# Optimization experiments

Hardware: AMD Instinct MI355X
Metric: run time of the kernel (lower is better)

## Reference

```python
import jax, jax.numpy as jnp
import numpy as np

WS = 8            # window size
N = WS * WS       # tokens per window
C = 192           # in_features
H = 6             # heads
HD = C // H       # head dim
MH = 256          # meta network hidden
BW = 4096         # batch_size * windows
NW_MASK = 64      # number of mask window patterns


def _relative_coords_log():
    idx = np.arange(WS)
    coords = np.stack(np.meshgrid(idx, idx, indexing='ij'), axis=0).reshape(2, -1)  # [2, N]
    rel = coords[:, :, None] - coords[:, None, :]            # [2, N, N]
    rel = rel.transpose(1, 2, 0).reshape(-1, 2).astype(np.float32)  # [N*N, 2]
    return jnp.asarray(np.sign(rel) * np.log1p(np.abs(rel)))


def setup_inputs() -> dict:
    key = jax.random.key(0)
    ks = jax.random.split(key, 12)
    s = 0.02
    return {
        'x': jax.random.normal(ks[0], (BW, C, WS, WS), jnp.float32),
        'mask': jax.random.normal(ks[1], (NW_MASK, N, N), jnp.float32),
        'W_qkv': jax.random.normal(ks[2], (C, 3 * C), jnp.float32) * s,
        'b_qkv': jnp.zeros((3 * C,), jnp.float32),
        'W_proj': jax.random.normal(ks[3], (C, C), jnp.float32) * s,
        'b_proj': jnp.zeros((C,), jnp.float32),
        'mW1': jax.random.normal(ks[4], (2, MH), jnp.float32) * 0.1,
        'mb1': jnp.zeros((MH,), jnp.float32),
        'mW2': jax.random.normal(ks[5], (MH, H), jnp.float32) * 0.1,
        'mb2': jnp.zeros((H,), jnp.float32),
        'tau': jnp.ones((H,), jnp.float32),
    }


def _l2norm(v):
    n = jnp.sqrt(jnp.sum(v * v, axis=-1, keepdims=True))
    return v / jnp.maximum(n, 1e-12)


def reference(x, mask, W_qkv, b_qkv, W_proj, b_proj, mW1, mb1, mW2, mb2, tau):
    Bw = x.shape[0]
    # [Bw, C, ws, ws] -> tokens [Bw, N, C]
    tokens = x.reshape(Bw, C, N).transpose(0, 2, 1)
    qkv = tokens @ W_qkv + b_qkv                                  # [Bw, N, 3C]
    qkv = qkv.reshape(Bw, N, 3, H, HD).transpose(2, 0, 3, 1, 4)   # [3, Bw, H, N, HD]
    q, k, v = qkv[0], qkv[1], qkv[2]
    # scaled cosine attention
    attn = jnp.einsum('bhnd,bhmd->bhnm', _l2norm(q), _l2norm(k))
    attn = attn / jnp.clip(tau, 0.01, None)[None, :, None, None]
    # continuous relative position bias via meta network
    rel_log = _relative_coords_log()                              # [N*N, 2]
    bias = jax.nn.relu(rel_log @ mW1 + mb1) @ mW2 + mb2           # [N*N, H]
    bias = bias.T.reshape(H, N, N)
    attn = attn + bias[None]
    # shifted-window mask, pattern indexed by window id modulo nW_mask
    idx = jnp.arange(Bw) % mask.shape[0]
    attn = attn + mask[idx][:, None]                              # [Bw, 1, N, N]
    attn = jax.nn.softmax(attn, axis=-1)
    out = jnp.einsum('bhnm,bhmd->bhnd', attn, v)
    out = out.transpose(0, 2, 1, 3).reshape(Bw, N, C)
    out = out @ W_proj + b_proj
    # back to [Bw, C, ws, ws]
    return out.transpose(0, 2, 1).reshape(Bw, C, WS, WS)
```

## Files before the change

kernel.cpp:

```cpp
#include <hip/hip_runtime.h>

typedef _Float16 f16;
typedef _Float16 f16x2 __attribute__((ext_vector_type(2)));
typedef _Float16 f16x4 __attribute__((ext_vector_type(4)));
typedef _Float16 f16x8 __attribute__((ext_vector_type(8)));
typedef float f32x4 __attribute__((ext_vector_type(4)));

#define NT 64
#define CH 192
#define NH 6
#define MH 256
#define BWIN 4096
#define LOG2E 1.44269504f

#define STOK 200
#define SMEM_BYTES 49152

#define MFMA16(a, b, c) __builtin_amdgcn_mfma_f32_16x16x16f16(a, b, c, 0, 0, 0)
#define MFMA32(a, b, c) __builtin_amdgcn_mfma_f32_16x16x32_f16(a, b, c, 0, 0, 0)

__device__ __forceinline__ int qkidx(int n, int d) {
    return n * 32 + ((((d >> 3) + (n >> 1)) & 3) << 3) + (d & 7);
}

__global__ void bias_kernel(const float* __restrict__ mW1, const float* __restrict__ mb1,
                            const float* __restrict__ mW2, const float* __restrict__ mb2,
                            float* __restrict__ bias_tbl) {
    int p = blockIdx.x * blockDim.x + threadIdx.x;
    if (p >= NT * NT) return;
    int n = p >> 6, m = p & 63;
    float di = (float)((n >> 3) - (m >> 3));
    float dj = (float)((n & 7) - (m & 7));
    float r0 = copysignf(log1pf(fabsf(di)), di);
    float r1 = copysignf(log1pf(fabsf(dj)), dj);
    float acc[NH];
#pragma unroll
    for (int h = 0; h < NH; h++) acc[h] = mb2[h];
    for (int k = 0; k < MH; k++) {
        float hv = fmaxf(r0 * mW1[k] + r1 * mW1[MH + k] + mb1[k], 0.0f);
#pragma unroll
        for (int h = 0; h < NH; h++) acc[h] += hv * mW2[k * NH + h];
    }
#pragma unroll
    for (int h = 0; h < NH; h++) bias_tbl[h * (NT * NT) + p] = acc[h];
}

__global__ void prep_kernel(const float* __restrict__ Wqkv, const float* __restrict__ Wproj,
                            f16* __restrict__ Wpk, f16* __restrict__ Wpp) {
    int i = blockIdx.x * blockDim.x + threadIdx.x;
    const int NQ = 36 * 6 * 64 * 8;
    if (i < NQ) {
        int t = i & 7, lane = (i >> 3) & 63, ks = (i >> 9) % 6, ct = i >> 9; ct /= 6;
        int o = 16 * ct + (lane & 15);
        int c = ks * 32 + (lane >> 4) * 8 + t;
        Wpk[i] = (f16)Wqkv[c * 576 + o];
    } else if (i < NQ + 12 * 6 * 64 * 8) {
        int j = i - NQ;
        int t = j & 7, lane = (j >> 3) & 63, ks = (j >> 9) % 6, ct = j >> 9; ct /= 6;
        int o = 16 * ct + (lane & 15);
        int c = ks * 32 + (lane >> 4) * 8 + t;
        Wpp[j] = (f16)Wproj[c * 192 + o];
    }
}

__global__ void comb_kernel(const float* __restrict__ mask, const float* __restrict__ bias_tbl,
                            float* __restrict__ comb) {
    int j = blockIdx.x * blockDim.x + threadIdx.x;
    if (j >= 64 * NH * NT * NT) return;
    int im = j / (NH * NT * NT);
    int rem = j % (NH * NT * NT);
    int h = rem >> 12;
    int p = rem & 4095;
    comb[j] = (mask[im * 4096 + p] + bias_tbl[h * 4096 + p]) * LOG2E;
}

__launch_bounds__(384)
__global__ void attn_kernel(const float* __restrict__ x, const float* __restrict__ bqkv,
                            const float* __restrict__ bproj, const float* __restrict__ tau,
                            const f16* __restrict__ Wpk, const f16* __restrict__ Wpp,
                            const float* __restrict__ comb, float* __restrict__ out) {
    __shared__ __align__(16) char smem[SMEM_BYTES];
    f16* tok = (f16*)smem;
    f16* qk  = (f16*)smem;
    f16* ao  = (f16*)smem;

    const int b   = blockIdx.x;
    const int tid = threadIdx.x;
    const int l   = tid & 63;
    const int w   = __builtin_amdgcn_readfirstlane(tid >> 6);
    const int c16 = l & 15;
    const int g4  = l >> 4;

    {
        const float* xb = x + (size_t)b * (CH * NT);
        const int n4 = 4 * c16;
#pragma unroll
        for (int i = 0; i < 4; i++) {
            int c = 32 * w + 8 * g4 + 2 * i;
            f32x4 a0 = *(const f32x4*)(xb + c * NT + n4);
            f32x4 a1 = *(const f32x4*)(xb + (c + 1) * NT + n4);
#pragma unroll
            for (int j = 0; j < 4; j++) {
                f16x2 p;
                p[0] = (f16)a0[j];
                p[1] = (f16)a1[j];
                *(f16x2*)(tok + (n4 + j) * STOK + c) = p;
            }
        }
    }
    __syncthreads();

    f16x4 hq[2][4], hk[2][4];
    {
        f32x4 aq_[2][4] = {};
#pragma unroll
        for (int ks = 0; ks < 6; ks++) {
            f16x8 af[4];
#pragma unroll
            for (int nt = 0; nt < 4; nt++)
                af[nt] = *(const f16x8*)(tok + (16 * nt + c16) * STOK + ks * 32 + 8 * g4);
#pragma unroll
            for (int dt = 0; dt < 2; dt++) {
                f16x8 wf = *(const f16x8*)(Wpk + (((size_t)(2 * w + dt) * 6 + ks) * 64 + l) * 8);
#pragma unroll
                for (int nt = 0; nt < 4; nt++)
                    aq_[dt][nt] = MFMA32(wf, af[nt], aq_[dt][nt]);
            }
        }
#pragma unroll
        for (int dt = 0; dt < 2; dt++) {
            f32x4 bb = *(const f32x4*)(bqkv + 32 * w + 16 * dt + 4 * g4);
#pragma unroll
            for (int nt = 0; nt < 4; nt++)
#pragma unroll
                for (int r = 0; r < 4; r++) aq_[dt][nt][r] += bb[r];
        }
#pragma unroll
        for (int nt = 0; nt < 4; nt++) {
            float ss = 0.f;
#pragma unroll
            for (int dt = 0; dt < 2; dt++)
#pragma unroll
                for (int r = 0; r < 4; r++) ss += aq_[dt][nt][r] * aq_[dt][nt][r];
            ss += __shfl_xor(ss, 16);
            ss += __shfl_xor(ss, 32);
            float iq = 1.0f / fmaxf(sqrtf(ss), 1e-12f);
#pragma unroll
            for (int dt = 0; dt < 2; dt++)
#pragma unroll
                for (int r = 0; r < 4; r++) hq[dt][nt][r] = (f16)(aq_[dt][nt][r] * iq);
        }
    }
    {
        f32x4 ak_[2][4] = {};
#pragma unroll
        for (int ks = 0; ks < 6; ks++) {
            f16x8 af[4];
#pragma unroll
            for (int nt = 0; nt < 4; nt++)
                af[nt] = *(const f16x8*)(tok + (16 * nt + c16) * STOK + ks * 32 + 8 * g4);
#pragma unroll
            for (int dt = 0; dt < 2; dt++) {
                f16x8 wf = *(const f16x8*)(Wpk + (((size_t)(12 + 2 * w + dt) * 6 + ks) * 64 + l) * 8);
#pragma unroll
                for (int nt = 0; nt < 4; nt++)
                    ak_[dt][nt] = MFMA32(wf, af[nt], ak_[dt][nt]);
            }
        }
#pragma unroll
        for (int dt = 0; dt < 2; dt++) {
            f32x4 bb = *(const f32x4*)(bqkv + 192 + 32 * w + 16 * dt + 4 * g4);
#pragma unroll
            for (int nt = 0; nt < 4; nt++)
#pragma unroll
                for (int r = 0; r < 4; r++) ak_[dt][nt][r] += bb[r];
        }
#pragma unroll
        for (int nt = 0; nt < 4; nt++) {
            float ss = 0.f;
#pragma unroll
            for (int dt = 0; dt < 2; dt++)
#pragma unroll
                for (int r = 0; r < 4; r++) ss += ak_[dt][nt][r] * ak_[dt][nt][r];
            ss += __shfl_xor(ss, 16);
            ss += __shfl_xor(ss, 32);
            float ik = 1.0f / fmaxf(sqrtf(ss), 1e-12f);
#pragma unroll
            for (int dt = 0; dt < 2; dt++)
#pragma unroll
                for (int r = 0; r < 4; r++) hk[dt][nt][r] = (f16)(ak_[dt][nt][r] * ik);
        }
    }
    f16x4 vb[2][4];
    {
        f32x4 av_[2][4] = {};
#pragma unroll
        for (int ks = 0; ks < 6; ks++) {
            f16x8 af[4];
#pragma unroll
            for (int mt = 0; mt < 4; mt++)
                af[mt] = *(const f16x8*)(tok + (16 * mt + c16) * STOK + ks * 32 + 8 * g4);
#pragma unroll
            for (int dt = 0; dt < 2; dt++) {
                f16x8 wf = *(const f16x8*)(Wpk + (((size_t)(24 + 2 * w + dt) * 6 + ks) * 64 + l) * 8);
#pragma unroll
                for (int mt = 0; mt < 4; mt++)
                    av_[dt][mt] = MFMA32(af[mt], wf, av_[dt][mt]);
            }
        }
#pragma unroll
        for (int dt = 0; dt < 2; dt++) {
            float bb = bqkv[384 + 32 * w + 16 * dt + c16];
#pragma unroll
            for (int mt = 0; mt < 4; mt++)
#pragma unroll
                for (int r = 0; r < 4; r++) vb[dt][mt][r] = (f16)(av_[dt][mt][r] + bb);
        }
    }

    __syncthreads();

    f16* qh = qk + (w * 2 + 0) * 2048;
    f16* kh = qk + (w * 2 + 1) * 2048;
#pragma unroll
    for (int nt = 0; nt < 4; nt++)
#pragma unroll
        for (int dt = 0; dt < 2; dt++) {
            int base = qkidx(16 * nt + c16, 16 * dt + 4 * g4);
            f16x2 p;
            p[0] = hq[dt][nt][0]; p[1] = hq[dt][nt][1];
            *(f16x2*)(qh + base) = p;
            p[0] = hq[dt][nt][2]; p[1] = hq[dt][nt][3];
            *(f16x2*)(qh + base + 2) = p;
            p[0] = hk[dt][nt][0]; p[1] = hk[dt][nt][1];
            *(f16x2*)(kh + base) = p;
            p[0] = hk[dt][nt][2]; p[1] = hk[dt][nt][3];
            *(f16x2*)(kh + base + 2) = p;
        }

    f32x4 sv[4][4];
    {
        f16x8 aqf[4];
#pragma unroll
        for (int t = 0; t < 4; t++)
            aqf[t] = *(const f16x8*)(qh + qkidx(16 * t + c16, 8 * g4));
#pragma unroll
        for (int mt = 0; mt < 4; mt++) {
            f16x8 akf = *(const f16x8*)(kh + qkidx(16 * mt + c16, 8 * g4));
#pragma unroll
            for (int nt = 0; nt < 4; nt++) {
                f32x4 z = {};
                sv[mt][nt] = MFMA32(akf, aqf[nt], z);
            }
        }
    }

    {
        const float itau_l2 = LOG2E / fmaxf(tau[w], 0.01f);
        const float* cb = comb + ((size_t)((b & 63) * NH + w)) * (NT * NT);
#pragma unroll
        for (int mt = 0; mt < 4; mt++)
#pragma unroll
            for (int nt = 0; nt < 4; nt++) {
                f32x4 cc = *(const f32x4*)(cb + (16 * nt + c16) * NT + 16 * mt + 4 * g4);
#pragma unroll
                for (int r = 0; r < 4; r++)
                    sv[mt][nt][r] = sv[mt][nt][r] * itau_l2 + cc[r];
            }
    }

#pragma unroll
    for (int nt = 0; nt < 4; nt++) {
        float mx = sv[0][nt][0];
#pragma unroll
        for (int mt = 0; mt < 4; mt++)
#pragma unroll
            for (int r = 0; r < 4; r++) mx = fmaxf(mx, sv[mt][nt][r]);
        mx = fmaxf(mx, __shfl_xor(mx, 16));
        mx = fmaxf(mx, __shfl_xor(mx, 32));
        float sum = 0.f;
#pragma unroll
        for (int mt = 0; mt < 4; mt++)
#pragma unroll
            for (int r = 0; r < 4; r++) {
                float p = exp2f(sv[mt][nt][r] - mx);
                sv[mt][nt][r] = p;
                sum += p;
            }
        sum += __shfl_xor(sum, 16);
        sum += __shfl_xor(sum, 32);
        float ris = 1.0f / sum;
#pragma unroll
        for (int mt = 0; mt < 4; mt++)
#pragma unroll
            for (int r = 0; r < 4; r++) sv[mt][nt][r] *= ris;
    }

    f16x4 pa[4][4];
#pragma unroll
    for (int mk = 0; mk < 4; mk++)
#pragma unroll
        for (int nt = 0; nt < 4; nt++) {
            f16x4 h;
#pragma unroll
            for (int r = 0; r < 4; r++) h[r] = (f16)sv[mk][nt][r];
            pa[mk][nt] = h;
        }

    f32x4 av[4][2] = {};
#pragma unroll
    for (int mk = 0; mk < 4; mk++)
#pragma unroll
        for (int nt = 0; nt < 4; nt++)
#pragma unroll
            for (int dt = 0; dt < 2; dt++)
                av[nt][dt] = MFMA16(pa[mk][nt], vb[dt][mk], av[nt][dt]);

    __syncthreads();

#pragma unroll
    for (int nt = 0; nt < 4; nt++)
#pragma unroll
        for (int dt = 0; dt < 2; dt++)
#pragma unroll
            for (int r = 0; r < 4; r++)
                ao[(16 * nt + 4 * g4 + r) * STOK + 32 * w + 16 * dt + c16] = (f16)av[nt][dt][r];
    __syncthreads();

    f32x4 acc2[2][4] = {};
#pragma unroll
    for (int ks = 0; ks < 6; ks++) {
        f16x8 af[4];
#pragma unroll
        for (int rt = 0; rt < 4; rt++)
            af[rt] = *(const f16x8*)(ao + (16 * rt + c16) * STOK + ks * 32 + 8 * g4);
#pragma unroll
        for (int c2 = 0; c2 < 2; c2++) {
            f16x8 bw = *(const f16x8*)(Wpp + (((size_t)(2 * w + c2) * 6 + ks) * 64 + l) * 8);
#pragma unroll
            for (int rt = 0; rt < 4; rt++)
                acc2[c2][rt] = MFMA32(af[rt], bw, acc2[c2][rt]);
        }
    }
    float* ob = out + (size_t)b * (CH * NT);
#pragma unroll
    for (int c2 = 0; c2 < 2; c2++) {
        int c = 16 * (2 * w + c2) + c16;
        float bp = bproj[c];
#pragma unroll
        for (int rt = 0; rt < 4; rt++) {
            f32x4 o4 = acc2[c2][rt];
            o4[0] += bp; o4[1] += bp; o4[2] += bp; o4[3] += bp;
            *(f32x4*)(ob + c * NT + 16 * rt + 4 * g4) = o4;
        }
    }
}

#define WS_BIAS 0
#define WS_WPK  98304
#define WS_WPP  319488
#define WS_COMB 393216

extern "C" void kernel_launch(void* const* d_in, const int* in_sizes, int n_in,
                              void* d_out, int out_size, void* d_ws, size_t ws_size,
                              hipStream_t stream) {
    const float* x     = (const float*)d_in[0];
    const float* mask  = (const float*)d_in[1];
    const float* Wqkv  = (const float*)d_in[2];
    const float* bqkv  = (const float*)d_in[3];
    const float* Wproj = (const float*)d_in[4];
    const float* bproj = (const float*)d_in[5];
    const float* mW1   = (const float*)d_in[6];
    const float* mb1   = (const float*)d_in[7];
    const float* mW2   = (const float*)d_in[8];
    const float* mb2   = (const float*)d_in[9];
    const float* tau   = (const float*)d_in[10];

    char* ws = (char*)d_ws;
    float* bias_tbl = (float*)(ws + WS_BIAS);
    f16*   Wpk      = (f16*)(ws + WS_WPK);
    f16*   Wpp      = (f16*)(ws + WS_WPP);
    float* comb     = (float*)(ws + WS_COMB);

    bias_kernel<<<16, 256, 0, stream>>>(mW1, mb1, mW2, mb2, bias_tbl);
    int prep_n = 36 * 6 * 64 * 8 + 12 * 6 * 64 * 8;
    prep_kernel<<<(prep_n + 255) / 256, 256, 0, stream>>>(Wqkv, Wproj, Wpk, Wpp);
    int comb_n = 64 * NH * NT * NT;
    comb_kernel<<<(comb_n + 255) / 256, 256, 0, stream>>>(mask, bias_tbl, comb);
    attn_kernel<<<BWIN, 384, 0, stream>>>(x, bqkv, bproj, tau, Wpk, Wpp, comb,
                                          (float*)d_out);
}
```

Before: 338.4 us.

## Process two windows per block to reuse weight fragments across windows

```diff
diff --git a/kernel.cpp b/kernel.cpp
--- a/kernel.cpp
+++ b/kernel.cpp
@@ -14,7 +14,8 @@
 #define LOG2E 1.44269504f
 
 #define STOK 200
-#define SMEM_BYTES 49152
+#define WIN_BYTES 49152
+#define SMEM_BYTES (2 * WIN_BYTES)
 
 #define MFMA16(a, b, c) __builtin_amdgcn_mfma_f32_16x16x16f16(a, b, c, 0, 0, 0)
 #define MFMA32(a, b, c) __builtin_amdgcn_mfma_f32_16x16x32_f16(a, b, c, 0, 0, 0)
@@ -74,284 +75,291 @@
     comb[j] = (mask[im * 4096 + p] + bias_tbl[h * 4096 + p]) * LOG2E;
 }
 
+template <bool TRANS>
+__device__ __forceinline__ void qkv_pass(const f16* tokA, const f16* tokB,
+                                         const f16* __restrict__ Wpk, int ctbase,
+                                         int c16, int g4, int l,
+                                         f32x4 (&accA)[2][4], f32x4 (&accB)[2][4]) {
+#pragma unroll
+    for (int ks = 0; ks < 6; ks++) {
+        f16x8 afA[4], afB[4];
+#pragma unroll
+        for (int nt = 0; nt < 4; nt++) {
+            afA[nt] = *(const f16x8*)(tokA + (16 * nt + c16) * STOK + ks * 32 + 8 * g4);
+            afB[nt] = *(const f16x8*)(tokB + (16 * nt + c16) * STOK + ks * 32 + 8 * g4);
+        }
+#pragma unroll
+        for (int dt = 0; dt < 2; dt++) {
+            f16x8 wf = *(const f16x8*)(Wpk + (((size_t)(ctbase + dt) * 6 + ks) * 64 + l) * 8);
+#pragma unroll
+            for (int nt = 0; nt < 4; nt++) {
+                if (TRANS) {
+                    accA[dt][nt] = MFMA32(wf, afA[nt], accA[dt][nt]);
+                    accB[dt][nt] = MFMA32(wf, afB[nt], accB[dt][nt]);
+                } else {
+                    accA[dt][nt] = MFMA32(afA[nt], wf, accA[dt][nt]);
+                    accB[dt][nt] = MFMA32(afB[nt], wf, accB[dt][nt]);
+                }
+            }
+        }
+    }
+}
+
+__device__ __forceinline__ void norm_pack(const f32x4 (&acc)[2][4], const float* __restrict__ bq,
+                                          int w, int g4, f16x4 (&h)[2][4]) {
+    f32x4 bb0 = *(const f32x4*)(bq + 32 * w + 4 * g4);
+    f32x4 bb1 = *(const f32x4*)(bq + 32 * w + 16 + 4 * g4);
+#pragma unroll
+    for (int nt = 0; nt < 4; nt++) {
+        float a0[4], a1[4];
+        float ss = 0.f;
+#pragma unroll
+        for (int r = 0; r < 4; r++) {
+            a0[r] = acc[0][nt][r] + bb0[r];
+            a1[r] = acc[1][nt][r] + bb1[r];
+            ss += a0[r] * a0[r] + a1[r] * a1[r];
+        }
+        ss += __shfl_xor(ss, 16);
+        ss += __shfl_xor(ss, 32);
+        float inv = 1.0f / fmaxf(sqrtf(ss), 1e-12f);
+#pragma unroll
+        for (int r = 0; r < 4; r++) {
+            h[0][nt][r] = (f16)(a0[r] * inv);
+            h[1][nt][r] = (f16)(a1[r] * inv);
+        }
+    }
+}
+
+__device__ __forceinline__ void attn_one(const f16* qh, const f16* kh,
+                                         const float* __restrict__ cb, float itau_l2,
+                                         const f16x4 (&vb)[2][4], int c16, int g4,
+                                         f32x4 (&av)[4][2]) {
+    f32x4 sv[4][4];
+    {
+        f16x8 aqf[4];
+#pragma unroll
+        for (int t = 0; t < 4; t++)
+            aqf[t] = *(const f16x8*)(qh + qkidx(16 * t + c16, 8 * g4));
+#pragma unroll
+        for (int mt = 0; mt < 4; mt++) {
+            f16x8 akf = *(const f16x8*)(kh + qkidx(16 * mt + c16, 8 * g4));
+#pragma unroll
+            for (int nt = 0; nt < 4; nt++) {
+                f32x4 z = {};
+                sv[mt][nt] = MFMA32(akf, aqf[nt], z);
+            }
+        }
+    }
+#pragma unroll
+    for (int mt = 0; mt < 4; mt++)
+#pragma unroll
+        for (int nt = 0; nt < 4; nt++) {
+            f32x4 cc = *(const f32x4*)(cb + (16 * nt + c16) * NT + 16 * mt + 4 * g4);
+#pragma unroll
+            for (int r = 0; r < 4; r++)
+                sv[mt][nt][r] = sv[mt][nt][r] * itau_l2 + cc[r];
+        }
+#pragma unroll
+    for (int nt = 0; nt < 4; nt++) {
+        float mx = sv[0][nt][0];
+#pragma unroll
+        for (int mt = 0; mt < 4; mt++)
+#pragma unroll
+            for (int r = 0; r < 4; r++) mx = fmaxf(mx, sv[mt][nt][r]);
+        mx = fmaxf(mx, __shfl_xor(mx, 16));
+        mx = fmaxf(mx, __shfl_xor(mx, 32));
+        float sum = 0.f;
+#pragma unroll
+        for (int mt = 0; mt < 4; mt++)
+#pragma unroll
+            for (int r = 0; r < 4; r++) {
+                float p = exp2f(sv[mt][nt][r] - mx);
+                sv[mt][nt][r] = p;
+                sum += p;
+            }
+        sum += __shfl_xor(sum, 16);
+        sum += __shfl_xor(sum, 32);
+        float ris = 1.0f / sum;
+#pragma unroll
+        for (int mt = 0; mt < 4; mt++)
+#pragma unroll
+            for (int r = 0; r < 4; r++) sv[mt][nt][r] *= ris;
+    }
+    f16x4 pa[4][4];
+#pragma unroll
+    for (int mk = 0; mk < 4; mk++)
+#pragma unroll
+        for (int nt = 0; nt < 4; nt++) {
+            f16x4 h;
+#pragma unroll
+            for (int r = 0; r < 4; r++) h[r] = (f16)sv[mk][nt][r];
+            pa[mk][nt] = h;
+        }
+#pragma unroll
+    for (int nt = 0; nt < 4; nt++)
+#pragma unroll
+        for (int dt = 0; dt < 2; dt++) {
+            f32x4 z = {};
+            av[nt][dt] = z;
+        }
+#pragma unroll
+    for (int mk = 0; mk < 4; mk++)
+#pragma unroll
+        for (int nt = 0; nt < 4; nt++)
+#pragma unroll
+            for (int dt = 0; dt < 2; dt++)
+                av[nt][dt] = MFMA16(pa[mk][nt], vb[dt][mk], av[nt][dt]);
+}
+
 __launch_bounds__(384)
 __global__ void attn_kernel(const float* __restrict__ x, const float* __restrict__ bqkv,
                             const float* __restrict__ bproj, const float* __restrict__ tau,
                             const f16* __restrict__ Wpk, const f16* __restrict__ Wpp,
                             const float* __restrict__ comb, float* __restrict__ out) {
     __shared__ __align__(16) char smem[SMEM_BYTES];
-    f16* tok = (f16*)smem;
-    f16* qk  = (f16*)smem;
-    f16* ao  = (f16*)smem;
-
-    const int b   = blockIdx.x;
+
     const int tid = threadIdx.x;
     const int l   = tid & 63;
     const int w   = __builtin_amdgcn_readfirstlane(tid >> 6);
+    const int b0  = blockIdx.x * 2;
+    const int b1  = b0 + 1;
     const int c16 = l & 15;
     const int g4  = l >> 4;
 
+    f16* tokA = (f16*)smem;
+    f16* tokB = (f16*)(smem + WIN_BYTES);
+    f16* qkA  = tokA;
+    f16* qkB  = tokB;
+    f16* aoA  = tokA;
+    f16* aoB  = tokB;
+
     {
-        const float* xb = x + (size_t)b * (CH * NT);
         const int n4 = 4 * c16;
 #pragma unroll
-        for (int i = 0; i < 4; i++) {
-            int c = 32 * w + 8 * g4 + 2 * i;
-            f32x4 a0 = *(const f32x4*)(xb + c * NT + n4);
-            f32x4 a1 = *(const f32x4*)(xb + (c + 1) * NT + n4);
-#pragma unroll
-            for (int j = 0; j < 4; j++) {
-                f16x2 p;
-                p[0] = (f16)a0[j];
-                p[1] = (f16)a1[j];
-                *(f16x2*)(tok + (n4 + j) * STOK + c) = p;
+        for (int wp = 0; wp < 2; wp++) {
+            const float* xb = x + (size_t)(b0 + wp) * (CH * NT);
+            f16* tok = wp ? tokB : tokA;
+#pragma unroll
+            for (int i = 0; i < 4; i++) {
+                int c = 32 * w + 8 * g4 + 2 * i;
+                f32x4 a0 = *(const f32x4*)(xb + c * NT + n4);
+                f32x4 a1 = *(const f32x4*)(xb + (c + 1) * NT + n4);
+#pragma unroll
+                for (int j = 0; j < 4; j++) {
+                    f16x2 p;
+                    p[0] = (f16)a0[j];
+                    p[1] = (f16)a1[j];
+                    *(f16x2*)(tok + (n4 + j) * STOK + c) = p;
+                }
             }
         }
     }
     __syncthreads();
 
-    f16x4 hq[2][4], hk[2][4];
+    f16x4 hqA[2][4], hqB[2][4], hkA[2][4], hkB[2][4];
+    f16x4 vbA[2][4], vbB[2][4];
     {
-        f32x4 aq_[2][4] = {};
-#pragma unroll
-        for (int ks = 0; ks < 6; ks++) {
-            f16x8 af[4];
-#pragma unroll
-            for (int nt = 0; nt < 4; nt++)
-                af[nt] = *(const f16x8*)(tok + (16 * nt + c16) * STOK + ks * 32 + 8 * g4);
-#pragma unroll
-            for (int dt = 0; dt < 2; dt++) {
-                f16x8 wf = *(const f16x8*)(Wpk + (((size_t)(2 * w + dt) * 6 + ks) * 64 + l) * 8);
-#pragma unroll
-                for (int nt = 0; nt < 4; nt++)
-                    aq_[dt][nt] = MFMA32(wf, af[nt], aq_[dt][nt]);
-            }
-        }
-#pragma unroll
-        for (int dt = 0; dt < 2; dt++) {
-            f32x4 bb = *(const f32x4*)(bqkv + 32 * w + 16 * dt + 4 * g4);
-#pragma unroll
-            for (int nt = 0; nt < 4; nt++)
-#pragma unroll
-                for (int r = 0; r < 4; r++) aq_[dt][nt][r] += bb[r];
-        }
-#pragma unroll
-        for (int nt = 0; nt < 4; nt++) {
-            float ss = 0.f;
-#pragma unroll
-            for (int dt = 0; dt < 2; dt++)
-#pragma unroll
-                for (int r = 0; r < 4; r++) ss += aq_[dt][nt][r] * aq_[dt][nt][r];
-            ss += __shfl_xor(ss, 16);
-            ss += __shfl_xor(ss, 32);
-            float iq = 1.0f / fmaxf(sqrtf(ss), 1e-12f);
-#pragma unroll
-            for (int dt = 0; dt < 2; dt++)
-#pragma unroll
-                for (int r = 0; r < 4; r++) hq[dt][nt][r] = (f16)(aq_[dt][nt][r] * iq);
-        }
+        f32x4 accA[2][4] = {}, accB[2][4] = {};
+        qkv_pass<true>(tokA, tokB, Wpk, 2 * w, c16, g4, l, accA, accB);
+        norm_pack(accA, bqkv, w, g4, hqA);
+        norm_pack(accB, bqkv, w, g4, hqB);
     }
     {
-        f32x4 ak_[2][4] = {};
-#pragma unroll
-        for (int ks = 0; ks < 6; ks++) {
-            f16x8 af[4];
-#pragma unroll
-            for (int nt = 0; nt < 4; nt++)
-                af[nt] = *(const f16x8*)(tok + (16 * nt + c16) * STOK + ks * 32 + 8 * g4);
-#pragma unroll
-            for (int dt = 0; dt < 2; dt++) {
-                f16x8 wf = *(const f16x8*)(Wpk + (((size_t)(12 + 2 * w + dt) * 6 + ks) * 64 + l) * 8);
-#pragma unroll
-                for (int nt = 0; nt < 4; nt++)
-                    ak_[dt][nt] = MFMA32(wf, af[nt], ak_[dt][nt]);
-            }
-        }
-#pragma unroll
-        for (int dt = 0; dt < 2; dt++) {
-            f32x4 bb = *(const f32x4*)(bqkv + 192 + 32 * w + 16 * dt + 4 * g4);
-#pragma unroll
-            for (int nt = 0; nt < 4; nt++)
-#pragma unroll
-                for (int r = 0; r < 4; r++) ak_[dt][nt][r] += bb[r];
-        }
-#pragma unroll
-        for (int nt = 0; nt < 4; nt++) {
-            float ss = 0.f;
-#pragma unroll
-            for (int dt = 0; dt < 2; dt++)
-#pragma unroll
-                for (int r = 0; r < 4; r++) ss += ak_[dt][nt][r] * ak_[dt][nt][r];
-            ss += __shfl_xor(ss, 16);
-            ss += __shfl_xor(ss, 32);
-            float ik = 1.0f / fmaxf(sqrtf(ss), 1e-12f);
-#pragma unroll
-            for (int dt = 0; dt < 2; dt++)
-#pragma unroll
-                for (int r = 0; r < 4; r++) hk[dt][nt][r] = (f16)(ak_[dt][nt][r] * ik);
-        }
-    }
-    f16x4 vb[2][4];
+        f32x4 accA[2][4] = {}, accB[2][4] = {};
+        qkv_pass<true>(tokA, tokB, Wpk, 12 + 2 * w, c16, g4, l, accA, accB);
+        norm_pack(accA, bqkv + CH, w, g4, hkA);
+        norm_pack(accB, bqkv + CH, w, g4, hkB);
+    }
     {
-        f32x4 av_[2][4] = {};
-#pragma unroll
-        for (int ks = 0; ks < 6; ks++) {
-            f16x8 af[4];
-#pragma unroll
-            for (int mt = 0; mt < 4; mt++)
-                af[mt] = *(const f16x8*)(tok + (16 * mt + c16) * STOK + ks * 32 + 8 * g4);
-#pragma unroll
-            for (int dt = 0; dt < 2; dt++) {
-                f16x8 wf = *(const f16x8*)(Wpk + (((size_t)(24 + 2 * w + dt) * 6 + ks) * 64 + l) * 8);
-#pragma unroll
-                for (int mt = 0; mt < 4; mt++)
-                    av_[dt][mt] = MFMA32(af[mt], wf, av_[dt][mt]);
-            }
-        }
+        f32x4 accA[2][4] = {}, accB[2][4] = {};
+        qkv_pass<false>(tokA, tokB, Wpk, 24 + 2 * w, c16, g4, l, accA, accB);
 #pragma unroll
         for (int dt = 0; dt < 2; dt++) {
             float bb = bqkv[384 + 32 * w + 16 * dt + c16];
 #pragma unroll
             for (int mt = 0; mt < 4; mt++)
 #pragma unroll
-                for (int r = 0; r < 4; r++) vb[dt][mt][r] = (f16)(av_[dt][mt][r] + bb);
+                for (int r = 0; r < 4; r++) {
+                    vbA[dt][mt][r] = (f16)(accA[dt][mt][r] + bb);
+                    vbB[dt][mt][r] = (f16)(accB[dt][mt][r] + bb);
+                }
         }
     }
 
     __syncthreads();
 
-    f16* qh = qk + (w * 2 + 0) * 2048;
-    f16* kh = qk + (w * 2 + 1) * 2048;
+    f16* qhA = qkA + (w * 2 + 0) * 2048;
+    f16* khA = qkA + (w * 2 + 1) * 2048;
+    f16* qhB = qkB + (w * 2 + 0) * 2048;
+    f16* khB = qkB + (w * 2 + 1) * 2048;
 #pragma unroll
     for (int nt = 0; nt < 4; nt++)
 #pragma unroll
         for (int dt = 0; dt < 2; dt++) {
             int base = qkidx(16 * nt + c16, 16 * dt + 4 * g4);
-            f16x2 p;
-            p[0] = hq[dt][nt][0]; p[1] = hq[dt][nt][1];
-            *(f16x2*)(qh + base) = p;
-            p[0] = hq[dt][nt][2]; p[1] = hq[dt][nt][3];
-            *(f16x2*)(qh + base + 2) = p;
-            p[0] = hk[dt][nt][0]; p[1] = hk[dt][nt][1];
-            *(f16x2*)(kh + base) = p;
-            p[0] = hk[dt][nt][2]; p[1] = hk[dt][nt][3];
-            *(f16x2*)(kh + base + 2) = p;
-        }
-
-    f32x4 sv[4][4];
-    {
-        f16x8 aqf[4];
-#pragma unroll
-        for (int t = 0; t < 4; t++)
-            aqf[t] = *(const f16x8*)(qh + qkidx(16 * t + c16, 8 * g4));
-#pragma unroll
-        for (int mt = 0; mt < 4; mt++) {
-            f16x8 akf = *(const f16x8*)(kh + qkidx(16 * mt + c16, 8 * g4));
-#pragma unroll
-            for (int nt = 0; nt < 4; nt++) {
-                f32x4 z = {};
-                sv[mt][nt] = MFMA32(akf, aqf[nt], z);
-            }
-        }
-    }
-
-    {
-        const float itau_l2 = LOG2E / fmaxf(tau[w], 0.01f);
-        const float* cb = comb + ((size_t)((b & 63) * NH + w)) * (NT * NT);
-#pragma unroll
-        for (int mt = 0; mt < 4; mt++)
-#pragma unroll
-            for (int nt = 0; nt < 4; nt++) {
-                f32x4 cc = *(const f32x4*)(cb + (16 * nt + c16) * NT + 16 * mt + 4 * g4);
-#pragma unroll
-                for (int r = 0; r < 4; r++)
-                    sv[mt][nt][r] = sv[mt][nt][r] * itau_l2 + cc[r];
-            }
-    }
-
-#pragma unroll
-    for (int nt = 0; nt < 4; nt++) {
-        float mx = sv[0][nt][0];
-#pragma unroll
-        for (int mt = 0; mt < 4; mt++)
-#pragma unroll
-            for (int r = 0; r < 4; r++) mx = fmaxf(mx, sv[mt][nt][r]);
-        mx = fmaxf(mx, __shfl_xor(mx, 16));
-        mx = fmaxf(mx, __shfl_xor(mx, 32));
-        float sum = 0.f;
-#pragma unroll
-        for (int mt = 0; mt < 4; mt++)
+            *(f16x2*)(qhA + base)     = f16x2{hqA[dt][nt][0], hqA[dt][nt][1]};
+            *(f16x2*)(qhA + base + 2) = f16x2{hqA[dt][nt][2], hqA[dt][nt][3]};
+            *(f16x2*)(khA + base)     = f16x2{hkA[dt][nt][0], hkA[dt][nt][1]};
+            *(f16x2*)(khA + base + 2) = f16x2{hkA[dt][nt][2], hkA[dt][nt][3]};
+            *(f16x2*)(qhB + base)     = f16x2{hqB[dt][nt][0], hqB[dt][nt][1]};
+            *(f16x2*)(qhB + base + 2) = f16x2{hqB[dt][nt][2], hqB[dt][nt][3]};
+            *(f16x2*)(khB + base)     = f16x2{hkB[dt][nt][0], hkB[dt][nt][1]};
+            *(f16x2*)(khB + base + 2) = f16x2{hkB[dt][nt][2], hkB[dt][nt][3]};
+        }
+
+    const float itau_l2 = LOG2E / fmaxf(tau[w], 0.01f);
+    const float* cbA = comb + ((size_t)((b0 & 63) * NH + w)) * (NT * NT);
+    const float* cbB = comb + ((size_t)((b1 & 63) * NH + w)) * (NT * NT);
+    f32x4 avA[4][2], avB[4][2];
+    attn_one(qhA, khA, cbA, itau_l2, vbA, c16, g4, avA);
+    attn_one(qhB, khB, cbB, itau_l2, vbB, c16, g4, avB);
+
+    __syncthreads();
+
+#pragma unroll
+    for (int nt = 0; nt < 4; nt++)
+#pragma unroll
+        for (int dt = 0; dt < 2; dt++)
 #pragma unroll
             for (int r = 0; r < 4; r++) {
-                float p = exp2f(sv[mt][nt][r] - mx);
-                sv[mt][nt][r] = p;
-                sum += p;
-            }
-        sum += __shfl_xor(sum, 16);
-        sum += __shfl_xor(sum, 32);
-        float ris = 1.0f / sum;
-#pragma unroll
-        for (int mt = 0; mt < 4; mt++)
-#pragma unroll
-            for (int r = 0; r < 4; r++) sv[mt][nt][r] *= ris;
-    }
-
-    f16x4 pa[4][4];
-#pragma unroll
-    for (int mk = 0; mk < 4; mk++)
-#pragma unroll
-        for (int nt = 0; nt < 4; nt++) {
-            f16x4 h;
-#pragma unroll
-            for (int r = 0; r < 4; r++) h[r] = (f16)sv[mk][nt][r];
-            pa[mk][nt] = h;
-        }
-
-    f32x4 av[4][2] = {};
-#pragma unroll
-    for (int mk = 0; mk < 4; mk++)
-#pragma unroll
-        for (int nt = 0; nt < 4; nt++)
-#pragma unroll
-            for (int dt = 0; dt < 2; dt++)
-                av[nt][dt] = MFMA16(pa[mk][nt], vb[dt][mk], av[nt][dt]);
-
+                aoA[(16 * nt + 4 * g4 + r) * STOK + 32 * w + 16 * dt + c16] = (f16)avA[nt][dt][r];
+                aoB[(16 * nt + 4 * g4 + r) * STOK + 32 * w + 16 * dt + c16] = (f16)avB[nt][dt][r];
+            }
     __syncthreads();
 
-#pragma unroll
-    for (int nt = 0; nt < 4; nt++)
-#pragma unroll
-        for (int dt = 0; dt < 2; dt++)
-#pragma unroll
-            for (int r = 0; r < 4; r++)
-                ao[(16 * nt + 4 * g4 + r) * STOK + 32 * w + 16 * dt + c16] = (f16)av[nt][dt][r];
-    __syncthreads();
-
-    f32x4 acc2[2][4] = {};
+    f32x4 acc2A[2][4] = {}, acc2B[2][4] = {};
 #pragma unroll
     for (int ks = 0; ks < 6; ks++) {
-        f16x8 af[4];
-#pragma unroll
-        for (int rt = 0; rt < 4; rt++)
-            af[rt] = *(const f16x8*)(ao + (16 * rt + c16) * STOK + ks * 32 + 8 * g4);
+        f16x8 afA[4], afB[4];
+#pragma unroll
+        for (int rt = 0; rt < 4; rt++) {
+            afA[rt] = *(const f16x8*)(aoA + (16 * rt + c16) * STOK + ks * 32 + 8 * g4);
+            afB[rt] = *(const f16x8*)(aoB + (16 * rt + c16) * STOK + ks * 32 + 8 * g4);
+        }
 #pragma unroll
         for (int c2 = 0; c2 < 2; c2++) {
             f16x8 bw = *(const f16x8*)(Wpp + (((size_t)(2 * w + c2) * 6 + ks) * 64 + l) * 8);
 #pragma unroll
-            for (int rt = 0; rt < 4; rt++)
-                acc2[c2][rt] = MFMA32(af[rt], bw, acc2[c2][rt]);
-        }
-    }
-    float* ob = out + (size_t)b * (CH * NT);
+            for (int rt = 0; rt < 4; rt++) {
+                acc2A[c2][rt] = MFMA32(afA[rt], bw, acc2A[c2][rt]);
+                acc2B[c2][rt] = MFMA32(afB[rt], bw, acc2B[c2][rt]);
+            }
+        }
+    }
+    float* obA = out + (size_t)b0 * (CH * NT);
+    float* obB = out + (size_t)b1 * (CH * NT);
 #pragma unroll
     for (int c2 = 0; c2 < 2; c2++) {
         int c = 16 * (2 * w + c2) + c16;
         float bp = bproj[c];
 #pragma unroll
         for (int rt = 0; rt < 4; rt++) {
-            f32x4 o4 = acc2[c2][rt];
-            o4[0] += bp; o4[1] += bp; o4[2] += bp; o4[3] += bp;
-            *(f32x4*)(ob + c * NT + 16 * rt + 4 * g4) = o4;
+            f32x4 oA = acc2A[c2][rt];
+            f32x4 oB = acc2B[c2][rt];
+#pragma unroll
+            for (int r = 0; r < 4; r++) { oA[r] += bp; oB[r] += bp; }
+            *(f32x4*)(obA + c * NT + 16 * rt + 4 * g4) = oA;
+            *(f32x4*)(obB + c * NT + 16 * rt + 4 * g4) = oB;
         }
     }
 }
@@ -387,6 +395,6 @@
     prep_kernel<<<(prep_n + 255) / 256, 256, 0, stream>>>(Wqkv, Wproj, Wpk, Wpp);
     int comb_n = 64 * NH * NT * NT;
     comb_kernel<<<(comb_n + 255) / 256, 256, 0, stream>>>(mask, bias_tbl, comb);
-    attn_kernel<<<BWIN, 384, 0, stream>>>(x, bqkv, bproj, tau, Wpk, Wpp, comb,
-                                          (float*)d_out);
-}
+    attn_kernel<<<BWIN / 2, 384, 0, stream>>>(x, bqkv, bproj, tau, Wpk, Wpp, comb,
+                                              (float*)d_out);
+}
```

Result: slower. 414.5 us (+22.5%).

## Split each head across two waves with 768-thread blocks

Applied to the files above, without the earlier changes.

```diff
diff --git a/kernel.cpp b/kernel.cpp
--- a/kernel.cpp
+++ b/kernel.cpp
@@ -74,7 +74,7 @@
     comb[j] = (mask[im * 4096 + p] + bias_tbl[h * 4096 + p]) * LOG2E;
 }
 
-__launch_bounds__(384)
+__launch_bounds__(768)
 __global__ void attn_kernel(const float* __restrict__ x, const float* __restrict__ bqkv,
                             const float* __restrict__ bproj, const float* __restrict__ tau,
                             const f16* __restrict__ Wpk, const f16* __restrict__ Wpp,
@@ -84,10 +84,12 @@
     f16* qk  = (f16*)smem;
     f16* ao  = (f16*)smem;
 
-    const int b   = blockIdx.x;
     const int tid = threadIdx.x;
     const int l   = tid & 63;
-    const int w   = __builtin_amdgcn_readfirstlane(tid >> 6);
+    const int v   = __builtin_amdgcn_readfirstlane(tid >> 6);
+    const int w   = v >> 1;
+    const int h   = v & 1;
+    const int b   = blockIdx.x;
     const int c16 = l & 15;
     const int g4  = l >> 4;
 
@@ -95,8 +97,8 @@
         const float* xb = x + (size_t)b * (CH * NT);
         const int n4 = 4 * c16;
 #pragma unroll
-        for (int i = 0; i < 4; i++) {
-            int c = 32 * w + 8 * g4 + 2 * i;
+        for (int i = 0; i < 2; i++) {
+            int c = 16 * v + 4 * g4 + 2 * i;
             f32x4 a0 = *(const f32x4*)(xb + c * NT + n4);
             f32x4 a1 = *(const f32x4*)(xb + (c + 1) * NT + n4);
 #pragma unroll
@@ -110,94 +112,90 @@
     }
     __syncthreads();
 
-    f16x4 hq[2][4], hk[2][4];
-    {
-        f32x4 aq_[2][4] = {};
+    f16x4 hq[2][2], hk[2][2];
+    f16x4 vb[2][4];
+    {
+        f32x4 acc[2][2] = {};
+#pragma unroll
+        for (int ks = 0; ks < 6; ks++) {
+            f16x8 af[2];
+#pragma unroll
+            for (int ntl = 0; ntl < 2; ntl++)
+                af[ntl] = *(const f16x8*)(tok + (16 * (2 * h + ntl) + c16) * STOK + ks * 32 + 8 * g4);
+#pragma unroll
+            for (int dt = 0; dt < 2; dt++) {
+                f16x8 wf = *(const f16x8*)(Wpk + (((size_t)(2 * w + dt) * 6 + ks) * 64 + l) * 8);
+#pragma unroll
+                for (int ntl = 0; ntl < 2; ntl++)
+                    acc[dt][ntl] = MFMA32(wf, af[ntl], acc[dt][ntl]);
+            }
+        }
+        f32x4 bb0 = *(const f32x4*)(bqkv + 32 * w + 4 * g4);
+        f32x4 bb1 = *(const f32x4*)(bqkv + 32 * w + 16 + 4 * g4);
+#pragma unroll
+        for (int ntl = 0; ntl < 2; ntl++) {
+            float a0[4], a1[4];
+            float ss = 0.f;
+#pragma unroll
+            for (int r = 0; r < 4; r++) {
+                a0[r] = acc[0][ntl][r] + bb0[r];
+                a1[r] = acc[1][ntl][r] + bb1[r];
+                ss += a0[r] * a0[r] + a1[r] * a1[r];
+            }
+            ss += __shfl_xor(ss, 16);
+            ss += __shfl_xor(ss, 32);
+            float inv = 1.0f / fmaxf(sqrtf(ss), 1e-12f);
+#pragma unroll
+            for (int r = 0; r < 4; r++) {
+                hq[0][ntl][r] = (f16)(a0[r] * inv);
+                hq[1][ntl][r] = (f16)(a1[r] * inv);
+            }
+        }
+    }
+    {
+        f32x4 acc[2][2] = {};
+#pragma unroll
+        for (int ks = 0; ks < 6; ks++) {
+            f16x8 af[2];
+#pragma unroll
+            for (int ntl = 0; ntl < 2; ntl++)
+                af[ntl] = *(const f16x8*)(tok + (16 * (2 * h + ntl) + c16) * STOK + ks * 32 + 8 * g4);
+#pragma unroll
+            for (int dt = 0; dt < 2; dt++) {
+                f16x8 wf = *(const f16x8*)(Wpk + (((size_t)(12 + 2 * w + dt) * 6 + ks) * 64 + l) * 8);
+#pragma unroll
+                for (int ntl = 0; ntl < 2; ntl++)
+                    acc[dt][ntl] = MFMA32(wf, af[ntl], acc[dt][ntl]);
+            }
+        }
+        f32x4 bb0 = *(const f32x4*)(bqkv + CH + 32 * w + 4 * g4);
+        f32x4 bb1 = *(const f32x4*)(bqkv + CH + 32 * w + 16 + 4 * g4);
+#pragma unroll
+        for (int ntl = 0; ntl < 2; ntl++) {
+            float a0[4], a1[4];
+            float ss = 0.f;
+#pragma unroll
+            for (int r = 0; r < 4; r++) {
+                a0[r] = acc[0][ntl][r] + bb0[r];
+                a1[r] = acc[1][ntl][r] + bb1[r];
+                ss += a0[r] * a0[r] + a1[r] * a1[r];
+            }
+            ss += __shfl_xor(ss, 16);
+            ss += __shfl_xor(ss, 32);
+            float inv = 1.0f / fmaxf(sqrtf(ss), 1e-12f);
+#pragma unroll
+            for (int r = 0; r < 4; r++) {
+                hk[0][ntl][r] = (f16)(a0[r] * inv);
+                hk[1][ntl][r] = (f16)(a1[r] * inv);
+            }
+        }
+    }
+    {
+        f32x4 acc[2][4] = {};
 #pragma unroll
         for (int ks = 0; ks < 6; ks++) {
             f16x8 af[4];
 #pragma unroll
-            for (int nt = 0; nt < 4; nt++)
-                af[nt] = *(const f16x8*)(tok + (16 * nt + c16) * STOK + ks * 32 + 8 * g4);
-#pragma unroll
-            for (int dt = 0; dt < 2; dt++) {
-                f16x8 wf = *(const f16x8*)(Wpk + (((size_t)(2 * w + dt) * 6 + ks) * 64 + l) * 8);
-#pragma unroll
-                for (int nt = 0; nt < 4; nt++)
-                    aq_[dt][nt] = MFMA32(wf, af[nt], aq_[dt][nt]);
-            }
-        }
-#pragma unroll
-        for (int dt = 0; dt < 2; dt++) {
-            f32x4 bb = *(const f32x4*)(bqkv + 32 * w + 16 * dt + 4 * g4);
-#pragma unroll
-            for (int nt = 0; nt < 4; nt++)
-#pragma unroll
-                for (int r = 0; r < 4; r++) aq_[dt][nt][r] += bb[r];
-        }
-#pragma unroll
-        for (int nt = 0; nt < 4; nt++) {
-            float ss = 0.f;
-#pragma unroll
-            for (int dt = 0; dt < 2; dt++)
-#pragma unroll
-                for (int r = 0; r < 4; r++) ss += aq_[dt][nt][r] * aq_[dt][nt][r];
-            ss += __shfl_xor(ss, 16);
-            ss += __shfl_xor(ss, 32);
-            float iq = 1.0f / fmaxf(sqrtf(ss), 1e-12f);
-#pragma unroll
-            for (int dt = 0; dt < 2; dt++)
-#pragma unroll
-                for (int r = 0; r < 4; r++) hq[dt][nt][r] = (f16)(aq_[dt][nt][r] * iq);
-        }
-    }
-    {
-        f32x4 ak_[2][4] = {};
-#pragma unroll
-        for (int ks = 0; ks < 6; ks++) {
-            f16x8 af[4];
-#pragma unroll
-            for (int nt = 0; nt < 4; nt++)
-                af[nt] = *(const f16x8*)(tok + (16 * nt + c16) * STOK + ks * 32 + 8 * g4);
-#pragma unroll
-            for (int dt = 0; dt < 2; dt++) {
-                f16x8 wf = *(const f16x8*)(Wpk + (((size_t)(12 + 2 * w + dt) * 6 + ks) * 64 + l) * 8);
-#pragma unroll
-                for (int nt = 0; nt < 4; nt++)
-                    ak_[dt][nt] = MFMA32(wf, af[nt], ak_[dt][nt]);
-            }
-        }
-#pragma unroll
-        for (int dt = 0; dt < 2; dt++) {
-            f32x4 bb = *(const f32x4*)(bqkv + 192 + 32 * w + 16 * dt + 4 * g4);
-#pragma unroll
-            for (int nt = 0; nt < 4; nt++)
-#pragma unroll
-                for (int r = 0; r < 4; r++) ak_[dt][nt][r] += bb[r];
-        }
-#pragma unroll
-        for (int nt = 0; nt < 4; nt++) {
-            float ss = 0.f;
-#pragma unroll
-            for (int dt = 0; dt < 2; dt++)
-#pragma unroll
-                for (int r = 0; r < 4; r++) ss += ak_[dt][nt][r] * ak_[dt][nt][r];
-            ss += __shfl_xor(ss, 16);
-            ss += __shfl_xor(ss, 32);
-            float ik = 1.0f / fmaxf(sqrtf(ss), 1e-12f);
-#pragma unroll
-            for (int dt = 0; dt < 2; dt++)
-#pragma unroll
-                for (int r = 0; r < 4; r++) hk[dt][nt][r] = (f16)(ak_[dt][nt][r] * ik);
-        }
-    }
-    f16x4 vb[2][4];
-    {
-        f32x4 av_[2][4] = {};
-#pragma unroll
-        for (int ks = 0; ks < 6; ks++) {
-            f16x8 af[4];
-#pragma unroll
             for (int mt = 0; mt < 4; mt++)
                 af[mt] = *(const f16x8*)(tok + (16 * mt + c16) * STOK + ks * 32 + 8 * g4);
 #pragma unroll
@@ -205,7 +203,7 @@
                 f16x8 wf = *(const f16x8*)(Wpk + (((size_t)(24 + 2 * w + dt) * 6 + ks) * 64 + l) * 8);
 #pragma unroll
                 for (int mt = 0; mt < 4; mt++)
-                    av_[dt][mt] = MFMA32(af[mt], wf, av_[dt][mt]);
+                    acc[dt][mt] = MFMA32(af[mt], wf, acc[dt][mt]);
             }
         }
 #pragma unroll
@@ -214,142 +212,140 @@
 #pragma unroll
             for (int mt = 0; mt < 4; mt++)
 #pragma unroll
-                for (int r = 0; r < 4; r++) vb[dt][mt][r] = (f16)(av_[dt][mt][r] + bb);
-        }
-    }
-
-    __syncthreads();
-
-    f16* qh = qk + (w * 2 + 0) * 2048;
-    f16* kh = qk + (w * 2 + 1) * 2048;
-#pragma unroll
-    for (int nt = 0; nt < 4; nt++)
-#pragma unroll
-        for (int dt = 0; dt < 2; dt++) {
-            int base = qkidx(16 * nt + c16, 16 * dt + 4 * g4);
-            f16x2 p;
-            p[0] = hq[dt][nt][0]; p[1] = hq[dt][nt][1];
-            *(f16x2*)(qh + base) = p;
-            p[0] = hq[dt][nt][2]; p[1] = hq[dt][nt][3];
-            *(f16x2*)(qh + base + 2) = p;
-            p[0] = hk[dt][nt][0]; p[1] = hk[dt][nt][1];
-            *(f16x2*)(kh + base) = p;
-            p[0] = hk[dt][nt][2]; p[1] = hk[dt][nt][3];
-            *(f16x2*)(kh + base + 2) = p;
-        }
-
-    f32x4 sv[4][4];
-    {
-        f16x8 aqf[4];
-#pragma unroll
-        for (int t = 0; t < 4; t++)
-            aqf[t] = *(const f16x8*)(qh + qkidx(16 * t + c16, 8 * g4));
+                for (int r = 0; r < 4; r++) vb[dt][mt][r] = (f16)(acc[dt][mt][r] + bb);
+        }
+    }
+
+    __syncthreads();
+
+    {
+        f16* qh = qk + (w * 2 + 0) * 2048;
+        f16* kh = qk + (w * 2 + 1) * 2048;
+#pragma unroll
+        for (int ntl = 0; ntl < 2; ntl++)
+#pragma unroll
+            for (int dt = 0; dt < 2; dt++) {
+                int base = qkidx(16 * (2 * h + ntl) + c16, 16 * dt + 4 * g4);
+                *(f16x2*)(qh + base)     = f16x2{hq[dt][ntl][0], hq[dt][ntl][1]};
+                *(f16x2*)(qh + base + 2) = f16x2{hq[dt][ntl][2], hq[dt][ntl][3]};
+                *(f16x2*)(kh + base)     = f16x2{hk[dt][ntl][0], hk[dt][ntl][1]};
+                *(f16x2*)(kh + base + 2) = f16x2{hk[dt][ntl][2], hk[dt][ntl][3]};
+            }
+    }
+    __syncthreads();
+
+    f32x4 av[2][2];
+    {
+        const f16* qh = qk + (w * 2 + 0) * 2048;
+        const f16* kh = qk + (w * 2 + 1) * 2048;
+        f16x8 aqf[2];
+#pragma unroll
+        for (int ntl = 0; ntl < 2; ntl++)
+            aqf[ntl] = *(const f16x8*)(qh + qkidx(16 * (2 * h + ntl) + c16, 8 * g4));
+        f32x4 sv[4][2];
 #pragma unroll
         for (int mt = 0; mt < 4; mt++) {
             f16x8 akf = *(const f16x8*)(kh + qkidx(16 * mt + c16, 8 * g4));
 #pragma unroll
-            for (int nt = 0; nt < 4; nt++) {
+            for (int ntl = 0; ntl < 2; ntl++) {
                 f32x4 z = {};
-                sv[mt][nt] = MFMA32(akf, aqf[nt], z);
-            }
-        }
-    }
-
-    {
+                sv[mt][ntl] = MFMA32(akf, aqf[ntl], z);
+            }
+        }
         const float itau_l2 = LOG2E / fmaxf(tau[w], 0.01f);
         const float* cb = comb + ((size_t)((b & 63) * NH + w)) * (NT * NT);
 #pragma unroll
         for (int mt = 0; mt < 4; mt++)
 #pragma unroll
-            for (int nt = 0; nt < 4; nt++) {
-                f32x4 cc = *(const f32x4*)(cb + (16 * nt + c16) * NT + 16 * mt + 4 * g4);
+            for (int ntl = 0; ntl < 2; ntl++) {
+                f32x4 cc = *(const f32x4*)(cb + (16 * (2 * h + ntl) + c16) * NT + 16 * mt + 4 * g4);
 #pragma unroll
                 for (int r = 0; r < 4; r++)
-                    sv[mt][nt][r] = sv[mt][nt][r] * itau_l2 + cc[r];
-            }
-    }
-
-#pragma unroll
-    for (int nt = 0; nt < 4; nt++) {
-        float mx = sv[0][nt][0];
-#pragma unroll
-        for (int mt = 0; mt < 4; mt++)
-#pragma unroll
-            for (int r = 0; r < 4; r++) mx = fmaxf(mx, sv[mt][nt][r]);
-        mx = fmaxf(mx, __shfl_xor(mx, 16));
-        mx = fmaxf(mx, __shfl_xor(mx, 32));
-        float sum = 0.f;
-#pragma unroll
-        for (int mt = 0; mt < 4; mt++)
-#pragma unroll
-            for (int r = 0; r < 4; r++) {
-                float p = exp2f(sv[mt][nt][r] - mx);
-                sv[mt][nt][r] = p;
-                sum += p;
-            }
-        sum += __shfl_xor(sum, 16);
-        sum += __shfl_xor(sum, 32);
-        float ris = 1.0f / sum;
-#pragma unroll
-        for (int mt = 0; mt < 4; mt++)
-#pragma unroll
-            for (int r = 0; r < 4; r++) sv[mt][nt][r] *= ris;
-    }
-
-    f16x4 pa[4][4];
-#pragma unroll
-    for (int mk = 0; mk < 4; mk++)
-#pragma unroll
-        for (int nt = 0; nt < 4; nt++) {
-            f16x4 h;
-#pragma unroll
-            for (int r = 0; r < 4; r++) h[r] = (f16)sv[mk][nt][r];
-            pa[mk][nt] = h;
-        }
-
-    f32x4 av[4][2] = {};
-#pragma unroll
-    for (int mk = 0; mk < 4; mk++)
-#pragma unroll
-        for (int nt = 0; nt < 4; nt++)
-#pragma unroll
-            for (int dt = 0; dt < 2; dt++)
-                av[nt][dt] = MFMA16(pa[mk][nt], vb[dt][mk], av[nt][dt]);
-
-    __syncthreads();
-
-#pragma unroll
-    for (int nt = 0; nt < 4; nt++)
+                    sv[mt][ntl][r] = sv[mt][ntl][r] * itau_l2 + cc[r];
+            }
+#pragma unroll
+        for (int ntl = 0; ntl < 2; ntl++) {
+            float mx = sv[0][ntl][0];
+#pragma unroll
+            for (int mt = 0; mt < 4; mt++)
+#pragma unroll
+                for (int r = 0; r < 4; r++) mx = fmaxf(mx, sv[mt][ntl][r]);
+            mx = fmaxf(mx, __shfl_xor(mx, 16));
+            mx = fmaxf(mx, __shfl_xor(mx, 32));
+            float sum = 0.f;
+#pragma unroll
+            for (int mt = 0; mt < 4; mt++)
+#pragma unroll
+                for (int r = 0; r < 4; r++) {
+                    float p = exp2f(sv[mt][ntl][r] - mx);
+                    sv[mt][ntl][r] = p;
+                    sum += p;
+                }
+            sum += __shfl_xor(sum, 16);
+            sum += __shfl_xor(sum, 32);
+            float ris = 1.0f / sum;
+#pragma unroll
+            for (int mt = 0; mt < 4; mt++)
+#pragma unroll
+                for (int r = 0; r < 4; r++) sv[mt][ntl][r] *= ris;
+        }
+        f16x4 pa[4][2];
+#pragma unroll
+        for (int mk = 0; mk < 4; mk++)
+#pragma unroll
+            for (int ntl = 0; ntl < 2; ntl++) {
+                f16x4 hh;
+#pragma unroll
+                for (int r = 0; r < 4; r++) hh[r] = (f16)sv[mk][ntl][r];
+                pa[mk][ntl] = hh;
+            }
+#pragma unroll
+        for (int ntl = 0; ntl < 2; ntl++)
+#pragma unroll
+            for (int dt = 0; dt < 2; dt++) {
+                f32x4 z = {};
+                av[ntl][dt] = z;
+            }
+#pragma unroll
+        for (int mk = 0; mk < 4; mk++)
+#pragma unroll
+            for (int ntl = 0; ntl < 2; ntl++)
+#pragma unroll
+                for (int dt = 0; dt < 2; dt++)
+                    av[ntl][dt] = MFMA16(pa[mk][ntl], vb[dt][mk], av[ntl][dt]);
+    }
+
+    __syncthreads();
+
+#pragma unroll
+    for (int ntl = 0; ntl < 2; ntl++)
 #pragma unroll
         for (int dt = 0; dt < 2; dt++)
 #pragma unroll
             for (int r = 0; r < 4; r++)
-                ao[(16 * nt + 4 * g4 + r) * STOK + 32 * w + 16 * dt + c16] = (f16)av[nt][dt][r];
-    __syncthreads();
-
-    f32x4 acc2[2][4] = {};
+                ao[(16 * (2 * h + ntl) + 4 * g4 + r) * STOK + 32 * w + 16 * dt + c16] =
+                    (f16)av[ntl][dt][r];
+    __syncthreads();
+
+    f32x4 acc2[4] = {};
 #pragma unroll
     for (int ks = 0; ks < 6; ks++) {
         f16x8 af[4];
 #pragma unroll
         for (int rt = 0; rt < 4; rt++)
             af[rt] = *(const f16x8*)(ao + (16 * rt + c16) * STOK + ks * 32 + 8 * g4);
-#pragma unroll
-        for (int c2 = 0; c2 < 2; c2++) {
-            f16x8 bw = *(const f16x8*)(Wpp + (((size_t)(2 * w + c2) * 6 + ks) * 64 + l) * 8);
-#pragma unroll
-            for (int rt = 0; rt < 4; rt++)
-                acc2[c2][rt] = MFMA32(af[rt], bw, acc2[c2][rt]);
-        }
+        f16x8 bw = *(const f16x8*)(Wpp + (((size_t)v * 6 + ks) * 64 + l) * 8);
+#pragma unroll
+        for (int rt = 0; rt < 4; rt++)
+            acc2[rt] = MFMA32(af[rt], bw, acc2[rt]);
     }
     float* ob = out + (size_t)b * (CH * NT);
-#pragma unroll
-    for (int c2 = 0; c2 < 2; c2++) {
-        int c = 16 * (2 * w + c2) + c16;
+    {
+        int c = 16 * v + c16;
         float bp = bproj[c];
 #pragma unroll
         for (int rt = 0; rt < 4; rt++) {
-            f32x4 o4 = acc2[c2][rt];
+            f32x4 o4 = acc2[rt];
             o4[0] += bp; o4[1] += bp; o4[2] += bp; o4[3] += bp;
             *(f32x4*)(ob + c * NT + 16 * rt + 4 * g4) = o4;
         }
@@ -387,6 +383,6 @@
     prep_kernel<<<(prep_n + 255) / 256, 256, 0, stream>>>(Wqkv, Wproj, Wpk, Wpp);
     int comb_n = 64 * NH * NT * NT;
     comb_kernel<<<(comb_n + 255) / 256, 256, 0, stream>>>(mask, bias_tbl, comb);
-    attn_kernel<<<BWIN, 384, 0, stream>>>(x, bqkv, bproj, tau, Wpk, Wpp, comb,
+    attn_kernel<<<BWIN, 768, 0, stream>>>(x, bqkv, bproj, tau, Wpk, Wpp, comb,
                                           (float*)d_out);
 }
```

Measured after the change: 389.4 us. 1.15x slower.
